# Optimization experiments

Measured on AMD Instinct MI355X. Metric: run time of the kernel, lower is better.

Reference implementation:

```python
import jax, jax.numpy as jnp
import numpy as np

N = 50000      # nodes
E = 640000     # edges
DIN = 128      # input feature dim
DOUT = 128     # env net output dim
DACT = 2       # action net output dim (keep/drop logits)
REL = 100      # relation embedding dim (hard-coded in get_net)
T = 2          # num edge types
TAU = 0.5      # gumbel temperature (CoGNN temp)


def _lin(k, i, o):
    return jax.random.normal(k, (o, i), jnp.float32) * np.float32(1.0 / np.sqrt(i))


def _hgn_params(key, din, dout):
    ks = jax.random.split(key, 5)
    return {"W_w": _lin(ks[0], din, dout), "W_b": jnp.zeros((dout,), jnp.float32),
            "Wr_w": _lin(ks[1], REL, dout), "Wr_b": jnp.zeros((dout,), jnp.float32),
            "a_w": _lin(ks[2], 3 * dout, 1), "a_b": jnp.zeros((1,), jnp.float32),
            "Wres_w": _lin(ks[3], din, dout), "Wres_b": jnp.zeros((dout,), jnp.float32),
            "rel_emb": jax.random.normal(ks[4], (T, REL), jnp.float32)}


def setup_inputs():
    key = jax.random.key(0)
    ks = jax.random.split(key, 8)
    inp = {"x": jax.random.normal(ks[0], (N, DIN), jnp.float32),
           "edge_index": jax.random.randint(ks[1], (2, E), 0, N, jnp.int32),
           "edge_type": jax.random.randint(ks[2], (E,), 0, T, jnp.int32)}
    u_in = jax.random.uniform(ks[3], (N, DACT), jnp.float32, 1e-6, 1.0 - 1e-6)
    u_out = jax.random.uniform(ks[4], (N, DACT), jnp.float32, 1e-6, 1.0 - 1e-6)
    inp["g_in"] = -jnp.log(-jnp.log(u_in))    # Gumbel(0,1) noise
    inp["g_out"] = -jnp.log(-jnp.log(u_out))
    for name, k, dout in (("inA", ks[5], DACT), ("outA", ks[6], DACT), ("env", ks[7], DOUT)):
        for pk, pv in _hgn_params(k, DIN, dout).items():
            inp[name + "_" + pk] = pv
    return inp


def _simple_hgn(x, src, dst, etype, W_w, W_b, Wr_w, Wr_b, a_w, a_b, Wres_w, Wres_b, rel_emb, mask=None):
    # out = scatter_add_dst( alpha_e * W x_src ) + W_res x   (SimpleHGN, add aggr)
    n = x.shape[0]
    dout = W_w.shape[0]
    h = x @ W_w.T + W_b                       # [N, dout] = W(x)
    r = rel_emb @ Wr_w.T + Wr_b               # [T, dout] = W_r(rel_emb)
    # a(cat(W(x_i), W(x_j), W_r(rel))) decomposed into three per-node/per-type dot products
    a1, a2, a3 = a_w[0, :dout], a_w[0, dout:2 * dout], a_w[0, 2 * dout:]
    s_dst = h @ a1                            # [N]
    s_src = h @ a2                            # [N]
    s_rel = r @ a3                            # [T]
    logits = jax.nn.leaky_relu(s_dst[dst] + s_src[src] + s_rel[etype] + a_b[0], 0.2)  # [E]
    if mask is not None:
        logits = jnp.where(mask, logits, -1e9)
    m = jax.ops.segment_max(logits, dst, num_segments=n)
    e = jnp.exp(logits - m[dst])
    if mask is not None:
        e = jnp.where(mask, e, 0.0)
    denom = jax.ops.segment_sum(e, dst, num_segments=n)
    alpha = e / jnp.maximum(denom[dst], 1e-16)   # edge softmax over incoming edges of each target
    aggr = jax.ops.segment_sum(h[src] * alpha[:, None], dst, num_segments=n)
    return aggr + x @ Wres_w.T + Wres_b


def _gumbel_hard(logits, g):
    y = jax.nn.softmax((logits + g) / TAU, axis=-1)
    y_hard = jax.nn.one_hot(jnp.argmax(y, axis=-1), y.shape[-1], dtype=y.dtype)
    return y_hard + y - jax.lax.stop_gradient(y)   # straight-through (hard=True)


def reference(x, edge_index, edge_type, g_in, g_out,
              inA_W_w, inA_W_b, inA_Wr_w, inA_Wr_b, inA_a_w, inA_a_b, inA_Wres_w, inA_Wres_b, inA_rel_emb,
              outA_W_w, outA_W_b, outA_Wr_w, outA_Wr_b, outA_a_w, outA_a_b, outA_Wres_w, outA_Wres_b, outA_rel_emb,
              env_W_w, env_W_b, env_Wr_w, env_Wr_b, env_a_w, env_a_b, env_Wres_w, env_Wres_b, env_rel_emb):
    src, dst = edge_index[0], edge_index[1]
    in_logits = _simple_hgn(x, src, dst, edge_type, inA_W_w, inA_W_b, inA_Wr_w, inA_Wr_b,
                            inA_a_w, inA_a_b, inA_Wres_w, inA_Wres_b, inA_rel_emb)
    out_logits = _simple_hgn(x, src, dst, edge_type, outA_W_w, outA_W_b, outA_Wr_w, outA_Wr_b,
                             outA_a_w, outA_a_b, outA_Wres_w, outA_Wres_b, outA_rel_emb)
    in_p = _gumbel_hard(in_logits, g_in)
    out_p = _gumbel_hard(out_logits, g_out)
    edge_weight = in_p[:, 0][dst] * out_p[:, 0][src]   # keep_in[v] * keep_out[u]
    mask = edge_weight > 0                              # hard edge filtering, non-differentiable as in torch
    return _simple_hgn(x, src, dst, edge_type, env_W_w, env_W_b, env_Wr_w, env_Wr_b,
                       env_a_w, env_a_b, env_Wres_w, env_Wres_b, env_rel_emb, mask=mask)
```

## Files before the change

kernel.cpp:

```cpp
#include <hip/hip_runtime.h>
#include <hip/hip_bf16.h>
#include <hip/hip_fp16.h>
#include <cstddef>

#define N_NODES 50000
#define N_EDGES 640000
#define DEG_CAP 48

__device__ __forceinline__ float lrelu(float z) { return z >= 0.f ? z : 0.2f * z; }

__device__ __forceinline__ unsigned short f2bf(float f) {
    unsigned u = __builtin_bit_cast(unsigned, f);
    u += 0x7FFFu + ((u >> 16) & 1u);
    return (unsigned short)(u >> 16);
}
__device__ __forceinline__ float bf2f(unsigned short h) {
    unsigned u = ((unsigned)h) << 16;
    return __builtin_bit_cast(float, u);
}

typedef __attribute__((ext_vector_type(8))) short short8;
typedef __attribute__((ext_vector_type(4))) float floatx4;

__global__ __launch_bounds__(256) void k_setup(
    const float* __restrict__ x,
    const float* __restrict__ rel_in, const float* __restrict__ Wr_in,
    const float* __restrict__ Wrb_in,
    const float* __restrict__ rel_out, const float* __restrict__ Wr_out,
    const float* __restrict__ Wrb_out,
    const float* __restrict__ rel_env, const float* __restrict__ Wr_env,
    const float* __restrict__ Wrb_env,
    const float* __restrict__ Wi, const float* __restrict__ Wib,
    const float* __restrict__ WiR, const float* __restrict__ WiRb,
    const float* __restrict__ ai,
    const float* __restrict__ Wo, const float* __restrict__ Wob,
    const float* __restrict__ WoR, const float* __restrict__ WoRb,
    const float* __restrict__ ao,
    const float* __restrict__ eW, const float* __restrict__ eWb,
    const float* __restrict__ eWR, const float* __restrict__ ea,
    float* __restrict__ srel,
    unsigned short* __restrict__ wh, unsigned short* __restrict__ wl,
    float4* __restrict__ dstT, float4* __restrict__ srcT,
    float4* __restrict__ h_pack, float4* __restrict__ res_pack)
{
    int b = blockIdx.x;
    int tid = threadIdx.x;

    if (b == 0) {
        __shared__ float red[256];
        __shared__ float rs[8];
        {
            int tt = tid >> 7, j = tid & 127;
            float acc = 0.f;
            for (int k = 0; k < 100; ++k) acc += rel_env[tt * 100 + k] * Wr_env[j * 100 + k];
            acc += Wrb_env[j];
            red[tid] = acc * ea[256 + j];
        }
        if (tid < 8) {
            int net = tid >> 2, tt = (tid >> 1) & 1, j = tid & 1;
            const float* re = net ? rel_out : rel_in;
            const float* wr = net ? Wr_out : Wr_in;
            const float* wb = net ? Wrb_out : Wrb_in;
            float acc = 0.f;
            for (int k = 0; k < 100; ++k) acc += re[tt * 100 + k] * wr[j * 100 + k];
            rs[tid] = acc + wb[j];
        }
        __syncthreads();
        if (tid < 2) {
            float s = 0.f;
            for (int j = 0; j < 128; ++j) s += red[tid * 128 + j];
            srel[4 + tid] = s;
        } else if (tid == 2) {
            srel[0] = rs[0] * ai[4] + rs[1] * ai[5];
            srel[1] = rs[2] * ai[4] + rs[3] * ai[5];
        } else if (tid == 3) {
            srel[2] = rs[4] * ao[4] + rs[5] * ao[5];
            srel[3] = rs[6] * ao[4] + rs[7] * ao[5];
        }
        return;
    }
    if (b < 129) {
        int i = (b - 1) * 256 + tid;
        float v = (i < 16384) ? eW[i] : eWR[i - 16384];
        unsigned short h = f2bf(v);
        wh[i] = h;
        wl[i] = f2bf(v - bf2f(h));
        return;
    }

    __shared__ float sw[10][128];
    __shared__ float vb[2];
    {
        int row = tid >> 5, c4 = tid & 31;
        const float* src;
        switch (row) {
            case 0: src = Wi;        break;
            case 1: src = Wi + 128;  break;
            case 2: src = WiR;       break;
            case 3: src = WiR + 128; break;
            case 4: src = Wo;        break;
            case 5: src = Wo + 128;  break;
            case 6: src = WoR;       break;
            default: src = WoR + 128; break;
        }
        float4 v = ((const float4*)src)[c4];
        sw[row][c4 * 4 + 0] = v.x; sw[row][c4 * 4 + 1] = v.y;
        sw[row][c4 * 4 + 2] = v.z; sw[row][c4 * 4 + 3] = v.w;
    }
    {
        int half = tid >> 7, k = tid & 127;
        const float* av = ea + half * 128;
        float s = 0.f;
        for (int j = 0; j < 128; ++j) s += eW[j * 128 + k] * av[j];
        sw[8 + half][k] = s;
    }
    if (tid < 2) {
        const float* av2 = ea + tid * 128;
        float sb = 0.f;
        for (int j = 0; j < 128; ++j) sb += eWb[j] * av2[j];
        vb[tid] = sb;
    }
    __syncthreads();
    int n = (b - 129) * 256 + tid;
    if (n >= N_NODES) return;
    const float4* xr = (const float4*)(x + (size_t)n * 128);
    float a0 = 0, a1 = 0, a2 = 0, a3 = 0, a4 = 0, a5 = 0, a6 = 0, a7 = 0;
    float a8 = 0, a9 = 0;
#pragma unroll 8
    for (int k4 = 0; k4 < 32; ++k4) {
        float4 v = xr[k4];
        int k = k4 * 4;
        a0 += v.x * sw[0][k] + v.y * sw[0][k + 1] + v.z * sw[0][k + 2] + v.w * sw[0][k + 3];
        a1 += v.x * sw[1][k] + v.y * sw[1][k + 1] + v.z * sw[1][k + 2] + v.w * sw[1][k + 3];
        a2 += v.x * sw[2][k] + v.y * sw[2][k + 1] + v.z * sw[2][k + 2] + v.w * sw[2][k + 3];
        a3 += v.x * sw[3][k] + v.y * sw[3][k + 1] + v.z * sw[3][k + 2] + v.w * sw[3][k + 3];
        a4 += v.x * sw[4][k] + v.y * sw[4][k + 1] + v.z * sw[4][k + 2] + v.w * sw[4][k + 3];
        a5 += v.x * sw[5][k] + v.y * sw[5][k + 1] + v.z * sw[5][k + 2] + v.w * sw[5][k + 3];
        a6 += v.x * sw[6][k] + v.y * sw[6][k + 1] + v.z * sw[6][k + 2] + v.w * sw[6][k + 3];
        a7 += v.x * sw[7][k] + v.y * sw[7][k + 1] + v.z * sw[7][k + 2] + v.w * sw[7][k + 3];
        a8 += v.x * sw[8][k] + v.y * sw[8][k + 1] + v.z * sw[8][k + 2] + v.w * sw[8][k + 3];
        a9 += v.x * sw[9][k] + v.y * sw[9][k + 1] + v.z * sw[9][k + 2] + v.w * sw[9][k + 3];
    }
    float hi0 = a0 + Wib[0], hi1 = a1 + Wib[1];
    float ri0 = a2 + WiRb[0], ri1 = a3 + WiRb[1];
    float ho0 = a4 + Wob[0], ho1 = a5 + Wob[1];
    float ro0 = a6 + WoRb[0], ro1 = a7 + WoRb[1];
    float sdi = hi0 * ai[0] + hi1 * ai[1];
    float ssi = hi0 * ai[2] + hi1 * ai[3];
    float sdo = ho0 * ao[0] + ho1 * ao[1];
    float sso = ho0 * ao[2] + ho1 * ao[3];
    dstT[n]     = make_float4(sdi, sdo, a8 + vb[0], 0.f);
    srcT[n]     = make_float4(ssi, sso, a9 + vb[1], 0.f);
    h_pack[n]   = make_float4(hi0, hi1, ho0, ho1);
    res_pack[n] = make_float4(ri0, ri1, ro0, ro1);
}

__global__ __launch_bounds__(256) void k_scatter(
    const int* __restrict__ ei, const int* __restrict__ et,
    const float4* __restrict__ dstT, const float4* __restrict__ srcT,
    const float* __restrict__ srel,
    const float* __restrict__ ab_in, const float* __restrict__ ab_out,
    const float* __restrict__ ab_env,
    int* __restrict__ cursor, int2* __restrict__ recsA, float2* __restrict__ sEin)
{
    int e = blockIdx.x * 256 + threadIdx.x;
    if (e >= N_EDGES) return;
    int src = ei[e], dst = ei[N_EDGES + e], t = et[e];
    float s0 = srel[0], s1 = srel[1], s2 = srel[2];
    float s3 = srel[3], s4 = srel[4], s5 = srel[5];
    float abi = ab_in[0], abo = ab_out[0], abe = ab_env[0];
    float4 dT = dstT[dst];
    float4 sT = srcT[src];
    float li = lrelu(dT.x + sT.x + (t ? s1 : s0) + abi);
    float lo = lrelu(dT.y + sT.y + (t ? s3 : s2) + abo);
    float le = lrelu(dT.z + sT.z + (t ? s5 : s4) + abe);
    int pos = atomicAdd(&cursor[dst], 1);
    if (pos < DEG_CAP) {
        int idx = dst * DEG_CAP + pos;
        recsA[idx] = make_int2(src, __float_as_int(__expf(le)));
        sEin[idx]  = make_float2(__expf(li), __expf(lo));
    }
}

__global__ __launch_bounds__(256) void k_action_seg(
    const int* __restrict__ cursor,
    const int2* __restrict__ recsA, const float2* __restrict__ sEin,
    const float4* __restrict__ h_pack, const float4* __restrict__ res_pack,
    const float* __restrict__ g_in, const float* __restrict__ g_out,
    unsigned char* __restrict__ flags)
{
    int gid = blockIdx.x * 256 + threadIdx.x;
    int n = gid >> 2, sub = gid & 3;
    if (n >= N_NODES) return;
    int cnt = min(cursor[n], DEG_CAP);
    int st = n * DEG_CAP;
    float ni0 = 0, ni1 = 0, di = 0, no0 = 0, no1 = 0, dob = 0;
    for (int i = sub; i < cnt; i += 4) {
        int2 r = recsA[st + i];
        float2 ee = sEin[st + i];
        float4 hp = h_pack[r.x];
        di  += ee.x; ni0 += ee.x * hp.x; ni1 += ee.x * hp.y;
        dob += ee.y; no0 += ee.y * hp.z; no1 += ee.y * hp.w;
    }
#pragma unroll
    for (int o = 1; o < 4; o <<= 1) {
        ni0 += __shfl_down(ni0, o); ni1 += __shfl_down(ni1, o);
        di  += __shfl_down(di,  o);
        no0 += __shfl_down(no0, o); no1 += __shfl_down(no1, o);
        dob += __shfl_down(dob, o);
    }
    if (sub == 0) {
        float4 rp = res_pack[n];
        float dinv = 1.f / fmaxf(di, 1e-16f);
        float l0 = ni0 * dinv + rp.x;
        float l1 = ni1 * dinv + rp.y;
        float2 gi = ((const float2*)g_in)[n];
        int in0 = (l0 + gi.x) >= (l1 + gi.y);
        float oinv = 1.f / fmaxf(dob, 1e-16f);
        float m0 = no0 * oinv + rp.z;
        float m1 = no1 * oinv + rp.w;
        float2 go = ((const float2*)g_out)[n];
        int out0 = (m0 + go.x) >= (m1 + go.y);
        flags[n] = (unsigned char)(in0 | (out0 << 1));
    }
}

__global__ __launch_bounds__(256, 2) void k_env_mfma(
    const float* __restrict__ x,
    const unsigned short* __restrict__ wh, const unsigned short* __restrict__ wl,
    const float* __restrict__ Wb, const float* __restrict__ WRb,
    __half* __restrict__ h_env, float* __restrict__ dout)
{
    int tid = threadIdx.x;
    int lane = tid & 63;
    int wv = tid >> 6;
    int l15 = lane & 15;
    int quad = lane >> 4;
    int jbase = wv * 64;

    short8 bh[4][4], bl[4][4];
    float bias[4];
#pragma unroll
    for (int jtl = 0; jtl < 4; ++jtl) {
        int j = jbase + jtl * 16 + l15;
        bias[jtl] = (j < 128) ? Wb[j] : WRb[j - 128];
#pragma unroll
        for (int ks = 0; ks < 4; ++ks) {
            size_t o = (size_t)j * 128 + ks * 32 + quad * 8;
            bh[jtl][ks] = *(const short8*)(wh + o);
            bl[jtl][ks] = *(const short8*)(wl + o);
        }
    }

    for (int t = blockIdx.x; t < 3125; t += gridDim.x) {
        int node = t * 16 + l15;
        const float4* ap = (const float4*)(x + (size_t)node * 128 + quad * 8);
        float4 f[8];
#pragma unroll
        for (int ks = 0; ks < 4; ++ks) {
            f[2 * ks]     = ap[ks * 8];
            f[2 * ks + 1] = ap[ks * 8 + 1];
        }
        short8 ah[4], al[4];
#pragma unroll
        for (int ks = 0; ks < 4; ++ks) {
            float av[8] = {f[2 * ks].x, f[2 * ks].y, f[2 * ks].z, f[2 * ks].w,
                           f[2 * ks + 1].x, f[2 * ks + 1].y, f[2 * ks + 1].z, f[2 * ks + 1].w};
#pragma unroll
            for (int i = 0; i < 8; ++i) {
                unsigned short h = f2bf(av[i]);
                ah[ks][i] = (short)h;
                al[ks][i] = (short)f2bf(av[i] - bf2f(h));
            }
        }
        floatx4 acc[4];
#pragma unroll
        for (int jtl = 0; jtl < 4; ++jtl) acc[jtl] = (floatx4)(0.f);
#pragma unroll
        for (int ks = 0; ks < 4; ++ks) {
#pragma unroll
            for (int jtl = 0; jtl < 4; ++jtl) {
                acc[jtl] = __builtin_amdgcn_mfma_f32_16x16x32_bf16(ah[ks], bh[jtl][ks], acc[jtl], 0, 0, 0);
                acc[jtl] = __builtin_amdgcn_mfma_f32_16x16x32_bf16(al[ks], bh[jtl][ks], acc[jtl], 0, 0, 0);
                acc[jtl] = __builtin_amdgcn_mfma_f32_16x16x32_bf16(ah[ks], bl[jtl][ks], acc[jtl], 0, 0, 0);
            }
        }
        int nb = t * 16 + quad * 4;
        if (wv < 2) {
#pragma unroll
            for (int jtl = 0; jtl < 4; ++jtl) {
                int j = jbase + jtl * 16 + l15;
#pragma unroll
                for (int r = 0; r < 4; ++r)
                    h_env[(size_t)(nb + r) * 128 + j] = __float2half(acc[jtl][r] + bias[jtl]);
            }
        } else {
#pragma unroll
            for (int jtl = 0; jtl < 4; ++jtl) {
                int j = jbase - 128 + jtl * 16 + l15;
#pragma unroll
                for (int r = 0; r < 4; ++r)
                    dout[(size_t)(nb + r) * 128 + j] = acc[jtl][r] + bias[jtl];
            }
        }
    }
}

__global__ __launch_bounds__(256) void k_aggr(
    const int* __restrict__ cursor,
    const int2* __restrict__ recsA, const unsigned char* __restrict__ flags,
    const __half* __restrict__ h_env, float* __restrict__ dout)
{
    __shared__ int   s_src[4][64];
    __shared__ float s_w[4][64];
    int tid = threadIdx.x;
    int lane = tid & 63;
    int wv = tid >> 6;
    int n = blockIdx.x * 4 + wv;
    if (n >= N_NODES) return;
    if (!(flags[n] & 1)) return;
    int cnt = min(cursor[n], DEG_CAP);
    int st = n * DEG_CAP;
    float ax = 0.f, ay = 0.f, den = 0.f;
    const __half2* h2 = (const __half2*)h_env;
    {
        int i = lane;
        bool act = false; int src = 0; float wgt = 0.f;
        if (i < cnt) {
            int2 r = recsA[st + i];
            src = r.x;
            wgt = __int_as_float(r.y);
            act = (flags[src] & 2) != 0;
        }
        unsigned long long bal = __ballot(act);
        int m = __popcll(bal);
        if (act) {
            int pos = __popcll(bal & ((1ull << lane) - 1));
            s_src[wv][pos] = src;
            s_w[wv][pos] = wgt;
        }
        __builtin_amdgcn_wave_barrier();
        int k = 0;
        for (; k + 4 <= m; k += 4) {
            int s0 = s_src[wv][k], s1 = s_src[wv][k + 1];
            int s2 = s_src[wv][k + 2], s3 = s_src[wv][k + 3];
            float w0 = s_w[wv][k], w1 = s_w[wv][k + 1];
            float w2 = s_w[wv][k + 2], w3 = s_w[wv][k + 3];
            float2 f0 = __half22float2(h2[(size_t)s0 * 64 + lane]);
            float2 f1 = __half22float2(h2[(size_t)s1 * 64 + lane]);
            float2 f2 = __half22float2(h2[(size_t)s2 * 64 + lane]);
            float2 f3 = __half22float2(h2[(size_t)s3 * 64 + lane]);
            den += (w0 + w1) + (w2 + w3);
            ax += w0 * f0.x + w1 * f1.x + w2 * f2.x + w3 * f3.x;
            ay += w0 * f0.y + w1 * f1.y + w2 * f2.y + w3 * f3.y;
        }
        for (; k < m; ++k) {
            int s0 = s_src[wv][k];
            float w0 = s_w[wv][k];
            float2 f0 = __half22float2(h2[(size_t)s0 * 64 + lane]);
            den += w0; ax += w0 * f0.x; ay += w0 * f0.y;
        }
    }
    float inv = 1.f / fmaxf(den, 1e-16f);
    float2* op = (float2*)dout + (size_t)n * 64 + lane;
    float2 r = *op;
    r.x = ax * inv + r.x;
    r.y = ay * inv + r.y;
    *op = r;
}

extern "C" void kernel_launch(void* const* d_in, const int* in_sizes, int n_in,
                              void* d_out, int out_size, void* d_ws, size_t ws_size,
                              hipStream_t stream)
{
    const float* x     = (const float*)d_in[0];
    const int*   ei    = (const int*)d_in[1];
    const int*   et    = (const int*)d_in[2];
    const float* g_in  = (const float*)d_in[3];
    const float* g_out = (const float*)d_in[4];
    const float* iW   = (const float*)d_in[5];
    const float* iWb  = (const float*)d_in[6];
    const float* iWr  = (const float*)d_in[7];
    const float* iWrb = (const float*)d_in[8];
    const float* ia   = (const float*)d_in[9];
    const float* iab  = (const float*)d_in[10];
    const float* iWR  = (const float*)d_in[11];
    const float* iWRb = (const float*)d_in[12];
    const float* irel = (const float*)d_in[13];
    const float* oW   = (const float*)d_in[14];
    const float* oWb  = (const float*)d_in[15];
    const float* oWr  = (const float*)d_in[16];
    const float* oWrb = (const float*)d_in[17];
    const float* oa   = (const float*)d_in[18];
    const float* oab  = (const float*)d_in[19];
    const float* oWR  = (const float*)d_in[20];
    const float* oWRb = (const float*)d_in[21];
    const float* orel = (const float*)d_in[22];
    const float* eW   = (const float*)d_in[23];
    const float* eWb  = (const float*)d_in[24];
    const float* eWr  = (const float*)d_in[25];
    const float* eWrb = (const float*)d_in[26];
    const float* ea   = (const float*)d_in[27];
    const float* eab  = (const float*)d_in[28];
    const float* eWR  = (const float*)d_in[29];
    const float* eWRb = (const float*)d_in[30];
    const float* erel = (const float*)d_in[31];
    float* dout = (float*)d_out;

    char* w = (char*)d_ws;
    size_t off = 0;
    auto alloc = [&](size_t bytes) -> char* {
        char* p = w + off;
        off += (bytes + 255) & ~(size_t)255;
        return p;
    };
    int*   cursor  = (int*)alloc((size_t)N_NODES * 4);
    size_t zeroBytes = off;
    float* srel    = (float*)alloc(16 * 4);
    float4* dstT     = (float4*)alloc((size_t)4 * N_NODES * 4);
    float4* srcT     = (float4*)alloc((size_t)4 * N_NODES * 4);
    float4* h_pack   = (float4*)alloc((size_t)4 * N_NODES * 4);
    float4* res_pack = (float4*)alloc((size_t)4 * N_NODES * 4);
    unsigned char* flags = (unsigned char*)alloc(N_NODES);
    unsigned short* wh = (unsigned short*)alloc((size_t)32768 * 2);
    unsigned short* wl = (unsigned short*)alloc((size_t)32768 * 2);
    int2*  recsA     = (int2*)alloc((size_t)N_NODES * DEG_CAP * 8);
    float2* sEin     = (float2*)alloc((size_t)N_NODES * DEG_CAP * 8);
    __half* h_env    = (__half*)alloc((size_t)N_NODES * 128 * 2);

    hipMemsetAsync(w, 0, zeroBytes, stream);
    k_setup<<<325, 256, 0, stream>>>(x,
                                     irel, iWr, iWrb, orel, oWr, oWrb, erel, eWr, eWrb,
                                     iW, iWb, iWR, iWRb, ia, oW, oWb, oWR, oWRb, oa,
                                     eW, eWb, eWR, ea,
                                     srel, wh, wl, dstT, srcT, h_pack, res_pack);
    k_scatter<<<2500, 256, 0, stream>>>(ei, et, dstT, srcT, srel, iab, oab, eab,
                                        cursor, recsA, sEin);
    k_env_mfma<<<512, 256, 0, stream>>>(x, wh, wl, eWb, eWRb, h_env, dout);
    k_action_seg<<<782, 256, 0, stream>>>(cursor, recsA, sEin, h_pack, res_pack,
                                          g_in, g_out, flags);
    k_aggr<<<12500, 256, 0, stream>>>(cursor, recsA, flags, h_env, dout);
}
```

Before: 244.5 us.

## Pack edge records and recompute action-net attention in segment kernel

The scatter kernel now writes a single 8-byte record per edge (src, edge type, env exp weight) instead of two 8-byte arrays, using a nontemporal store. The in/out action-net attention exponentials are recomputed in the per-node segment kernel from the dst and src scores. The src score and h_pack are interleaved into one srcPack array so both come from adjacent memory. This halves edge-record write traffic and the scatter's work, in exchange for extra gathers and exp evaluations in the action kernel. It assumes node ids fit in 20 bits.

```diff
diff --git a/kernel.cpp b/kernel.cpp
--- a/kernel.cpp
+++ b/kernel.cpp
@@ -40,8 +40,8 @@
     const float* __restrict__ eWR, const float* __restrict__ ea,
     float* __restrict__ srel,
     unsigned short* __restrict__ wh, unsigned short* __restrict__ wl,
-    float4* __restrict__ dstT, float4* __restrict__ srcT,
-    float4* __restrict__ h_pack, float4* __restrict__ res_pack)
+    float4* __restrict__ dstT, float4* __restrict__ srcPack,
+    float4* __restrict__ res_pack)
 {
     int b = blockIdx.x;
     int tid = threadIdx.x;
@@ -149,43 +149,41 @@
     float ssi = hi0 * ai[2] + hi1 * ai[3];
     float sdo = ho0 * ao[0] + ho1 * ao[1];
     float sso = ho0 * ao[2] + ho1 * ao[3];
-    dstT[n]     = make_float4(sdi, sdo, a8 + vb[0], 0.f);
-    srcT[n]     = make_float4(ssi, sso, a9 + vb[1], 0.f);
-    h_pack[n]   = make_float4(hi0, hi1, ho0, ho1);
-    res_pack[n] = make_float4(ri0, ri1, ro0, ro1);
+    dstT[n]           = make_float4(sdi, sdo, a8 + vb[0], 0.f);
+    srcPack[2 * n]     = make_float4(ssi, sso, a9 + vb[1], 0.f);
+    srcPack[2 * n + 1] = make_float4(hi0, hi1, ho0, ho1);
+    res_pack[n]       = make_float4(ri0, ri1, ro0, ro1);
 }
 
 __global__ __launch_bounds__(256) void k_scatter(
     const int* __restrict__ ei, const int* __restrict__ et,
-    const float4* __restrict__ dstT, const float4* __restrict__ srcT,
-    const float* __restrict__ srel,
-    const float* __restrict__ ab_in, const float* __restrict__ ab_out,
-    const float* __restrict__ ab_env,
-    int* __restrict__ cursor, int2* __restrict__ recsA, float2* __restrict__ sEin)
+    const float4* __restrict__ dstT, const float4* __restrict__ srcPack,
+    const float* __restrict__ srel, const float* __restrict__ ab_env,
+    int* __restrict__ cursor, unsigned long long* __restrict__ recs)
 {
     int e = blockIdx.x * 256 + threadIdx.x;
     if (e >= N_EDGES) return;
     int src = ei[e], dst = ei[N_EDGES + e], t = et[e];
-    float s0 = srel[0], s1 = srel[1], s2 = srel[2];
-    float s3 = srel[3], s4 = srel[4], s5 = srel[5];
-    float abi = ab_in[0], abo = ab_out[0], abe = ab_env[0];
+    float s4 = srel[4], s5 = srel[5];
+    float abe = ab_env[0];
     float4 dT = dstT[dst];
-    float4 sT = srcT[src];
-    float li = lrelu(dT.x + sT.x + (t ? s1 : s0) + abi);
-    float lo = lrelu(dT.y + sT.y + (t ? s3 : s2) + abo);
+    float4 sT = srcPack[2 * src];
     float le = lrelu(dT.z + sT.z + (t ? s5 : s4) + abe);
     int pos = atomicAdd(&cursor[dst], 1);
     if (pos < DEG_CAP) {
-        int idx = dst * DEG_CAP + pos;
-        recsA[idx] = make_int2(src, __float_as_int(__expf(le)));
-        sEin[idx]  = make_float2(__expf(li), __expf(lo));
+        unsigned lo = (unsigned)(src | (t << 20));
+        unsigned hi = (unsigned)__float_as_int(__expf(le));
+        unsigned long long rec = ((unsigned long long)hi << 32) | lo;
+        __builtin_nontemporal_store(rec, &recs[dst * DEG_CAP + pos]);
     }
 }
 
 __global__ __launch_bounds__(256) void k_action_seg(
-    const int* __restrict__ cursor,
-    const int2* __restrict__ recsA, const float2* __restrict__ sEin,
-    const float4* __restrict__ h_pack, const float4* __restrict__ res_pack,
+    const int* __restrict__ cursor, const unsigned long long* __restrict__ recs,
+    const float4* __restrict__ dstT, const float4* __restrict__ srcPack,
+    const float4* __restrict__ res_pack,
+    const float* __restrict__ srel,
+    const float* __restrict__ ab_in, const float* __restrict__ ab_out,
     const float* __restrict__ g_in, const float* __restrict__ g_out,
     unsigned char* __restrict__ flags)
 {
@@ -194,13 +192,21 @@
     if (n >= N_NODES) return;
     int cnt = min(cursor[n], DEG_CAP);
     int st = n * DEG_CAP;
+    float s0 = srel[0], s1 = srel[1], s2 = srel[2], s3 = srel[3];
+    float abi = ab_in[0], abo = ab_out[0];
+    float4 dT = dstT[n];
     float ni0 = 0, ni1 = 0, di = 0, no0 = 0, no1 = 0, dob = 0;
     for (int i = sub; i < cnt; i += 4) {
-        int2 r = recsA[st + i];
-        float2 ee = sEin[st + i];
-        float4 hp = h_pack[r.x];
-        di  += ee.x; ni0 += ee.x * hp.x; ni1 += ee.x * hp.y;
-        dob += ee.y; no0 += ee.y * hp.z; no1 += ee.y * hp.w;
+        unsigned long long rec = recs[st + i];
+        int src = (int)(rec & 0xFFFFFu);
+        int t = (int)((rec >> 20) & 0xFFFu);
+        float4 sT = srcPack[2 * src];
+        float4 hp = srcPack[2 * src + 1];
+        float li = lrelu(dT.x + sT.x + (t ? s1 : s0) + abi);
+        float lo = lrelu(dT.y + sT.y + (t ? s3 : s2) + abo);
+        float ein = __expf(li), eout = __expf(lo);
+        di  += ein;  ni0 += ein * hp.x;  ni1 += ein * hp.y;
+        dob += eout; no0 += eout * hp.z; no1 += eout * hp.w;
     }
 #pragma unroll
     for (int o = 1; o < 4; o <<= 1) {
@@ -308,7 +314,7 @@
 
 __global__ __launch_bounds__(256) void k_aggr(
     const int* __restrict__ cursor,
-    const int2* __restrict__ recsA, const unsigned char* __restrict__ flags,
+    const unsigned long long* __restrict__ recs, const unsigned char* __restrict__ flags,
     const __half* __restrict__ h_env, float* __restrict__ dout)
 {
     __shared__ int   s_src[4][64];
@@ -327,9 +333,9 @@
         int i = lane;
         bool act = false; int src = 0; float wgt = 0.f;
         if (i < cnt) {
-            int2 r = recsA[st + i];
-            src = r.x;
-            wgt = __int_as_float(r.y);
+            unsigned long long rec = recs[st + i];
+            src = (int)(rec & 0xFFFFFu);
+            wgt = __int_as_float((int)(rec >> 32));
             act = (flags[src] & 2) != 0;
         }
         unsigned long long bal = __ballot(act);
@@ -418,26 +424,24 @@
     size_t zeroBytes = off;
     float* srel    = (float*)alloc(16 * 4);
     float4* dstT     = (float4*)alloc((size_t)4 * N_NODES * 4);
-    float4* srcT     = (float4*)alloc((size_t)4 * N_NODES * 4);
-    float4* h_pack   = (float4*)alloc((size_t)4 * N_NODES * 4);
+    float4* srcPack  = (float4*)alloc((size_t)8 * N_NODES * 4);
     float4* res_pack = (float4*)alloc((size_t)4 * N_NODES * 4);
     unsigned char* flags = (unsigned char*)alloc(N_NODES);
     unsigned short* wh = (unsigned short*)alloc((size_t)32768 * 2);
     unsigned short* wl = (unsigned short*)alloc((size_t)32768 * 2);
-    int2*  recsA     = (int2*)alloc((size_t)N_NODES * DEG_CAP * 8);
-    float2* sEin     = (float2*)alloc((size_t)N_NODES * DEG_CAP * 8);
+    unsigned long long* recs = (unsigned long long*)alloc((size_t)N_NODES * DEG_CAP * 8);
     __half* h_env    = (__half*)alloc((size_t)N_NODES * 128 * 2);
 
-    hipMemsetAsync(w, 0, zeroBytes, stream);
+    (void)hipMemsetAsync(w, 0, zeroBytes, stream);
     k_setup<<<325, 256, 0, stream>>>(x,
                                      irel, iWr, iWrb, orel, oWr, oWrb, erel, eWr, eWrb,
                                      iW, iWb, iWR, iWRb, ia, oW, oWb, oWR, oWRb, oa,
                                      eW, eWb, eWR, ea,
-                                     srel, wh, wl, dstT, srcT, h_pack, res_pack);
-    k_scatter<<<2500, 256, 0, stream>>>(ei, et, dstT, srcT, srel, iab, oab, eab,
-                                        cursor, recsA, sEin);
+                                     srel, wh, wl, dstT, srcPack, res_pack);
+    k_scatter<<<2500, 256, 0, stream>>>(ei, et, dstT, srcPack, srel, eab,
+                                        cursor, recs);
     k_env_mfma<<<512, 256, 0, stream>>>(x, wh, wl, eWb, eWRb, h_env, dout);
-    k_action_seg<<<782, 256, 0, stream>>>(cursor, recsA, sEin, h_pack, res_pack,
-                                          g_in, g_out, flags);
-    k_aggr<<<12500, 256, 0, stream>>>(cursor, recsA, flags, h_env, dout);
-}
+    k_action_seg<<<782, 256, 0, stream>>>(cursor, recs, dstT, srcPack, res_pack,
+                                          srel, iab, oab, g_in, g_out, flags);
+    k_aggr<<<12500, 256, 0, stream>>>(cursor, recs, flags, h_env, dout);
+}
```

Result: no change. 246.8 us (+0.9%).
